# Kernel tuning notes

Measured on AMD Instinct MI355X. Metric: run time of the kernel, lower is better.

Reference implementation:

```python
import jax, jax.numpy as jnp
import numpy as np

EMBED_DIM = 1024
NUM_TOKENS = 32
TOKEN_DIM = 32  # ceil(1024/32)
CODEBOOK_SIZE = 256
BATCH = 32768
BETA = 0.25


def setup_inputs() -> dict:
    key = jax.random.key(0)
    ks = jax.random.split(key, 6)
    lim_e = 1.0 / np.sqrt(EMBED_DIM)
    lim_d = 1.0 / np.sqrt(NUM_TOKENS * TOKEN_DIM)
    lim_c = 1.0 / CODEBOOK_SIZE
    return {
        "skills": jax.random.normal(ks[0], (BATCH, EMBED_DIM), jnp.float32),
        "enc_w": jax.random.uniform(ks[1], (NUM_TOKENS * TOKEN_DIM, EMBED_DIM), jnp.float32, -lim_e, lim_e),
        "enc_b": jax.random.uniform(ks[2], (NUM_TOKENS * TOKEN_DIM,), jnp.float32, -lim_e, lim_e),
        "codebook": jax.random.uniform(ks[3], (CODEBOOK_SIZE, TOKEN_DIM), jnp.float32, -lim_c, lim_c),
        "dec_w": jax.random.uniform(ks[4], (EMBED_DIM, NUM_TOKENS * TOKEN_DIM), jnp.float32, -lim_d, lim_d),
        "dec_b": jax.random.uniform(ks[5], (EMBED_DIM,), jnp.float32, -lim_d, lim_d),
    }


def reference(skills, enc_w, enc_b, codebook, dec_w, dec_b):
    B = skills.shape[0]
    # encoder linear -> [B, num_tokens, token_dim]
    projected = (skills @ enc_w.T + enc_b).reshape(B, NUM_TOKENS, TOKEN_DIM)
    flat = projected.reshape(-1, TOKEN_DIM)  # [B*T, d]
    # squared-euclidean distances to codebook entries: [B*T, K]
    dists = (
        jnp.sum(flat * flat, axis=1, keepdims=True)
        - 2.0 * flat @ codebook.T
        + jnp.sum(codebook * codebook, axis=1)[None, :]
    )
    codes = jnp.argmin(dists, axis=1)  # [B*T]
    quantized = codebook[codes].reshape(B, NUM_TOKENS, TOKEN_DIM)
    # straight-through estimator
    st = projected + jax.lax.stop_gradient(quantized - projected)
    commitment = jnp.mean((projected - jax.lax.stop_gradient(quantized)) ** 2)
    codebook_loss = jnp.mean((quantized - jax.lax.stop_gradient(projected)) ** 2)
    vq_loss = codebook_loss + BETA * commitment
    reconstructed = st.reshape(B, NUM_TOKENS * TOKEN_DIM) @ dec_w.T + dec_b
    recon_loss = jnp.mean((reconstructed - skills) ** 2)
    loss = vq_loss + recon_loss
    return reconstructed, codes.reshape(B, NUM_TOKENS), loss
```

## Files before the change

kernel.cpp:

```cpp
#include <hip/hip_runtime.h>
#include <hip/hip_bf16.h>
#include <float.h>

#define OUT_CODES_OFF (33554432UL)
#define OUT_LOSS_OFF  (34603008UL)
#define TAU 1e-5f
#define INV_N (1.0f/33554432.0f)

typedef __attribute__((ext_vector_type(8))) short s16x8;
typedef __attribute__((ext_vector_type(4))) float f32x4;

__device__ __forceinline__ unsigned short bf16r(float x) {
    unsigned int u = __float_as_uint(x);
    unsigned int r = (u + 0x7FFFu + ((u >> 16) & 1u)) >> 16;
    return (unsigned short)r;
}
__device__ __forceinline__ float bf16f(unsigned short h) {
    return __uint_as_float(((unsigned int)h) << 16);
}
__device__ __forceinline__ void split8r(float4 v0, float4 v1, s16x8& h, s16x8& l) {
    float xs[8] = {v0.x, v0.y, v0.z, v0.w, v1.x, v1.y, v1.z, v1.w};
    #pragma unroll
    for (int e = 0; e < 8; ++e) {
        unsigned int u = __float_as_uint(xs[e]);
        unsigned short hh = (unsigned short)(u >> 16);
        h[e] = (short)hh;
        l[e] = (short)bf16r(xs[e] - bf16f(hh));
    }
}

__device__ __forceinline__ void gld16(const unsigned short* g, unsigned short* l) {
    __builtin_amdgcn_global_load_lds(
        (const __attribute__((address_space(1))) unsigned int*)g,
        (__attribute__((address_space(3))) unsigned int*)l, 16, 0, 0);
}

__global__ void k_prep_split(const float* __restrict__ in,
                             unsigned short* __restrict__ ot)
{
    const int b = blockIdx.x, tid = threadIdx.x;
    const int rblk = b >> 5, kt = b & 31, r = tid >> 2, q = tid & 3;
    const float* src = in + (size_t)(rblk * 128 + r) * 1024 + kt * 32 + q * 8;
    float4 v0 = *(const float4*)src, v1 = *(const float4*)(src + 4);
    s16x8 h, l;
    split8r(v0, v1, h, l);
    unsigned short* dst = ot + (size_t)b * 8192 + q * 1024 + r * 8;
    *(s16x8*)dst = h;
    *(s16x8*)(dst + 4096) = l;
}

__global__ void k_prep_r(const float* __restrict__ in,
                         unsigned short* __restrict__ o,
                         int n8)
{
    const int i = blockIdx.x * 256 + threadIdx.x;
    if (i >= n8) return;
    const float4* p = (const float4*)(in + (size_t)i * 8);
    float4 v0 = p[0], v1 = p[1];
    float xs[8] = {v0.x, v0.y, v0.z, v0.w, v1.x, v1.y, v1.z, v1.w};
    s16x8 h;
    #pragma unroll
    for (int e = 0; e < 8; ++e) h[e] = (short)bf16r(xs[e]);
    *(s16x8*)(o + (size_t)i * 8) = h;
}

__launch_bounds__(512, 1)
__global__ void k_enc_gl(const unsigned short* __restrict__ At,
                         const unsigned short* __restrict__ Bt,
                         const float* __restrict__ enc_b,
                         const float* __restrict__ cb_g,
                         float* __restrict__ out)
{
    __shared__ __align__(16) unsigned short us[49664];

    const int tid = threadIdx.x;
    const int wg = blockIdx.x;
    const int xcd = wg & 7, slot = wg >> 3;
    const int rb = xcd * 32 + (slot >> 1), chf = slot & 1;
    const int r0 = rb * 128;
    const int wid = tid >> 6, lane = tid & 63;
    const int wm = wid >> 1, wn = wid & 1;
    const int mbase = wm * 32;
    const int lhi = lane >> 4, llo = lane & 15;

    if (tid < 256) {
        const float4* cr = (const float4*)&cb_g[tid * 32];
        float s = 0.f;
        #pragma unroll
        for (int i = 0; i < 8; ++i) {
            float4 v = cr[i];
            float c[4] = {v.x, v.y, v.z, v.w};
            #pragma unroll
            for (int e = 0; e < 4; ++e) {
                const int d = i * 4 + e, kc = d >> 3, e8 = d & 7;
                unsigned int u = __float_as_uint(c[e]);
                unsigned short hh = (unsigned short)(u >> 16);
                us[32768 + kc * 2048 + tid * 8 + e8] = hh;
                us[40960 + kc * 2048 + tid * 8 + e8] = bf16r(c[e] - bf16f(hh));
                s = fmaf(c[e], c[e], s);
            }
        }
        *(float*)&us[49152 + tid * 2] = s;
    }
    {
        const unsigned short* gA = At + ((size_t)(rb * 32 + 0)) * 8192 + tid * 8;
        const unsigned short* gB = Bt + ((size_t)((chf * 4 + 0) * 32 + 0)) * 8192 + tid * 8;
        gld16(gA,        us + wid * 512);
        gld16(gA + 4096, us + 4096 + wid * 512);
        gld16(gB,        us + 8192 + wid * 512);
        gld16(gB + 4096, us + 12288 + wid * 512);
    }
    __syncthreads();

    float vq_local = 0.f;
    f32x4 acc[2][4];
    const int ntg_base = chf * 4;

    for (int it = 0; it < 128; ++it) {
        const int nt = it >> 5, kt = it & 31;
        if (kt == 0) {
            #pragma unroll
            for (int mf = 0; mf < 2; ++mf)
                #pragma unroll
                for (int nf = 0; nf < 4; ++nf) acc[mf][nf] = (f32x4)0.f;
        }
        if (it < 127) {
            const int tt = it + 1, ntn = tt >> 5, ktn = tt & 31;
            const int nb = (tt & 1) * 16384;
            const unsigned short* gA = At + ((size_t)(rb * 32 + ktn)) * 8192 + tid * 8;
            const unsigned short* gB = Bt + ((size_t)((ntg_base + ntn) * 32 + ktn)) * 8192 + tid * 8;
            gld16(gA,        us + nb + wid * 512);
            gld16(gA + 4096, us + nb + 4096 + wid * 512);
            gld16(gB,        us + nb + 8192 + wid * 512);
            gld16(gB + 4096, us + nb + 12288 + wid * 512);
        }
        {
            const int cb0 = (it & 1) * 16384;
            s16x8 ah[2], al[2];
            #pragma unroll
            for (int mf = 0; mf < 2; ++mf) {
                const int row = mbase + mf * 16 + llo;
                ah[mf] = *(s16x8*)&us[cb0 + lhi * 1024 + row * 8];
                al[mf] = *(s16x8*)&us[cb0 + 4096 + lhi * 1024 + row * 8];
            }
            #pragma unroll
            for (int nf = 0; nf < 4; ++nf) {
                const int rowb = wn * 64 + nf * 16 + llo;
                s16x8 bh = *(s16x8*)&us[cb0 + 8192 + lhi * 1024 + rowb * 8];
                s16x8 bl = *(s16x8*)&us[cb0 + 12288 + lhi * 1024 + rowb * 8];
                #pragma unroll
                for (int mf = 0; mf < 2; ++mf) {
                    acc[mf][nf] = __builtin_amdgcn_mfma_f32_16x16x32_bf16(ah[mf], bh, acc[mf][nf], 0, 0, 0);
                    acc[mf][nf] = __builtin_amdgcn_mfma_f32_16x16x32_bf16(ah[mf], bl, acc[mf][nf], 0, 0, 0);
                    acc[mf][nf] = __builtin_amdgcn_mfma_f32_16x16x32_bf16(al[mf], bh, acc[mf][nf], 0, 0, 0);
                }
            }
        }

        if (kt == 31) {
            for (int c = 0; c < 2; ++c) {
                __syncthreads();
                if (wn == c) {
                    #pragma unroll
                    for (int nf = 0; nf < 4; ++nf) {
                        const int colh = nf * 16 + llo;
                        const int tlc = colh >> 5, d = colh & 31;
                        const int kc = d >> 3, e8 = d & 7;
                        const float bias = enc_b[chf * 512 + nt * 128 + c * 64 + colh];
                        #pragma unroll
                        for (int mf = 0; mf < 2; ++mf)
                            #pragma unroll
                            for (int r = 0; r < 4; ++r) {
                                const int m_local = mbase + mf * 16 + lhi * 4 + r;
                                float val = acc[mf][nf][r] + bias;
                                unsigned int u = __float_as_uint(val);
                                unsigned short hh = (unsigned short)(u >> 16);
                                const int tok = m_local * 2 + tlc;
                                us[16384 + kc * 2048 + tok * 8 + e8] = hh;
                                us[24576 + kc * 2048 + tok * 8 + e8] = bf16r(val - bf16f(hh));
                            }
                    }
                }
                __syncthreads();
                s16x8 fh[2], fl[2];
                #pragma unroll
                for (int gi = 0; gi < 2; ++gi) {
                    const int tokrow = (wid * 2 + gi) * 16 + llo;
                    fh[gi] = *(s16x8*)&us[16384 + lhi * 2048 + tokrow * 8];
                    fl[gi] = *(s16x8*)&us[24576 + lhi * 2048 + tokrow * 8];
                }
                float s1[2][4], s2[2][4]; int bj[2][4];
                #pragma unroll
                for (int gi = 0; gi < 2; ++gi)
                    #pragma unroll
                    for (int r = 0; r < 4; ++r) { s1[gi][r] = FLT_MAX; s2[gi][r] = FLT_MAX; bj[gi][r] = 0; }
                for (int jb = 0; jb < 16; ++jb) {
                    const int j = jb * 16 + llo;
                    s16x8 ch = *(s16x8*)&us[32768 + lhi * 2048 + j * 8];
                    s16x8 cl = *(s16x8*)&us[40960 + lhi * 2048 + j * 8];
                    const float cnv = *(const float*)&us[49152 + j * 2];
                    #pragma unroll
                    for (int gi = 0; gi < 2; ++gi) {
                        f32x4 sc = (f32x4)0.f;
                        sc = __builtin_amdgcn_mfma_f32_16x16x32_bf16(fh[gi], ch, sc, 0, 0, 0);
                        sc = __builtin_amdgcn_mfma_f32_16x16x32_bf16(fh[gi], cl, sc, 0, 0, 0);
                        sc = __builtin_amdgcn_mfma_f32_16x16x32_bf16(fl[gi], ch, sc, 0, 0, 0);
                        #pragma unroll
                        for (int r = 0; r < 4; ++r) {
                            float s = fmaf(-2.f, sc[r], cnv);
                            if (s < s1[gi][r])      { s2[gi][r] = s1[gi][r]; s1[gi][r] = s; bj[gi][r] = j; }
                            else if (s < s2[gi][r]) { s2[gi][r] = s; }
                        }
                    }
                }
                #pragma unroll
                for (int gi = 0; gi < 2; ++gi) {
                    float Fp = 0.f;
                    #pragma unroll
                    for (int e = 0; e < 8; ++e) {
                        float fv = bf16f((unsigned short)fh[gi][e]) + bf16f((unsigned short)fl[gi][e]);
                        Fp = fmaf(fv, fv, Fp);
                    }
                    Fp += __shfl_xor(Fp, 16);
                    Fp += __shfl_xor(Fp, 32);
                    #pragma unroll
                    for (int r = 0; r < 4; ++r) {
                        float a1 = s1[gi][r], a2 = s2[gi][r]; int aj = bj[gi][r];
                        #pragma unroll
                        for (int off = 1; off <= 8; off <<= 1) {
                            float o1 = __shfl_xor(a1, off);
                            float o2 = __shfl_xor(a2, off);
                            int   oj = __shfl_xor(aj, off);
                            if (o1 < a1) { a2 = fminf(a1, o2); a1 = o1; aj = oj; }
                            else         { a2 = fminf(o1, a2); }
                        }
                        const float Ft = __shfl(Fp, lhi * 4 + r);
                        if (llo == 0) {
                            const int tok_local = (wid * 2 + gi) * 16 + lhi * 4 + r;
                            const int row = tok_local >> 1, tlc2 = tok_local & 1;
                            const int t = chf * 16 + nt * 4 + c * 2 + tlc2;
                            float cv = (a2 - a1 < TAU) ? (float)(aj + 512) : (float)aj;
                            out[OUT_CODES_OFF + (size_t)(r0 + row) * 32 + t] = cv;
                            vq_local += Ft + a1;
                        }
                    }
                }
            }
        }
        __syncthreads();
    }
    {
        float v = vq_local;
        #pragma unroll
        for (int off = 32; off >= 1; off >>= 1) v += __shfl_xor(v, off);
        if (lane == 0) atomicAdd(&out[OUT_LOSS_OFF], v * (1.25f * INV_N));
    }
}

__launch_bounds__(512, 1)
__global__ void k_enc_fb(const float* __restrict__ skills,
                         const float* __restrict__ enc_w,
                         const float* __restrict__ enc_b,
                         const float* __restrict__ cb_g,
                         float* __restrict__ out)
{
    __shared__ __align__(16) unsigned short us[40960];

    const int tid = threadIdx.x;
    const int rb = blockIdx.x >> 1, chf = blockIdx.x & 1;
    const int r0 = rb * 128;
    const int wid = tid >> 6, lane = tid & 63;
    const int wm = wid >> 1, wn = wid & 1;
    const int mbase = wm * 32;
    const int lhi = lane >> 4, llo = lane & 15;
    const int srow = tid >> 2, sq = tid & 3;

    if (tid < 256) {
        const float4* cr = (const float4*)&cb_g[tid * 32];
        float s = 0.f;
        #pragma unroll
        for (int i = 0; i < 8; ++i) {
            float4 v = cr[i];
            float c[4] = {v.x, v.y, v.z, v.w};
            #pragma unroll
            for (int e = 0; e < 4; ++e) {
                const int d = i * 4 + e;
                unsigned int u = __float_as_uint(c[e]);
                unsigned short hh = (unsigned short)(u >> 16);
                us[20480 + tid * 40 + d] = hh;
                us[30720 + tid * 40 + d] = bf16r(c[e] - bf16f(hh));
                s = fmaf(c[e], c[e], s);
            }
        }
        *(float*)&us[20480 + tid * 40 + 32] = s;
    }
    __syncthreads();

    float vq_local = 0.f;
    f32x4 acc[2][4];
    float4 ra0, ra1, rb0, rb1;
    {
        const float* ap = &skills[(size_t)(r0 + srow) * 1024 + sq * 8];
        ra0 = *(const float4*)ap; ra1 = *(const float4*)(ap + 4);
        const float* bp = &enc_w[(size_t)(chf * 512 + srow) * 1024 + sq * 8];
        rb0 = *(const float4*)bp; rb1 = *(const float4*)(bp + 4);
    }

    for (int it = 0; it < 128; ++it) {
        const int nt = it >> 5, kt = it & 31;
        if (kt == 0) {
            #pragma unroll
            for (int mf = 0; mf < 2; ++mf)
                #pragma unroll
                for (int nf = 0; nf < 4; ++nf) acc[mf][nf] = (f32x4)0.f;
        }
        __syncthreads();
        {
            s16x8 h, l;
            split8r(ra0, ra1, h, l);
            *(s16x8*)&us[srow * 40 + sq * 8] = h;
            *(s16x8*)&us[5120 + srow * 40 + sq * 8] = l;
            split8r(rb0, rb1, h, l);
            *(s16x8*)&us[10240 + srow * 40 + sq * 8] = h;
            *(s16x8*)&us[15360 + srow * 40 + sq * 8] = l;
        }
        __syncthreads();
        if (it < 127) {
            const int it2 = it + 1, nt2 = it2 >> 5, kt2 = it2 & 31;
            const float* ap = &skills[(size_t)(r0 + srow) * 1024 + kt2 * 32 + sq * 8];
            ra0 = *(const float4*)ap; ra1 = *(const float4*)(ap + 4);
            const float* bp = &enc_w[(size_t)(chf * 512 + nt2 * 128 + srow) * 1024 + kt2 * 32 + sq * 8];
            rb0 = *(const float4*)bp; rb1 = *(const float4*)(bp + 4);
        }
        {
            s16x8 ah[2], al[2];
            #pragma unroll
            for (int mf = 0; mf < 2; ++mf) {
                const int row = mbase + mf * 16 + llo;
                ah[mf] = *(s16x8*)&us[row * 40 + lhi * 8];
                al[mf] = *(s16x8*)&us[5120 + row * 40 + lhi * 8];
            }
            #pragma unroll
            for (int nf = 0; nf < 4; ++nf) {
                const int rowb = wn * 64 + nf * 16 + llo;
                s16x8 bh = *(s16x8*)&us[10240 + rowb * 40 + lhi * 8];
                s16x8 bl = *(s16x8*)&us[15360 + rowb * 40 + lhi * 8];
                #pragma unroll
                for (int mf = 0; mf < 2; ++mf) {
                    acc[mf][nf] = __builtin_amdgcn_mfma_f32_16x16x32_bf16(ah[mf], bh, acc[mf][nf], 0, 0, 0);
                    acc[mf][nf] = __builtin_amdgcn_mfma_f32_16x16x32_bf16(ah[mf], bl, acc[mf][nf], 0, 0, 0);
                    acc[mf][nf] = __builtin_amdgcn_mfma_f32_16x16x32_bf16(al[mf], bh, acc[mf][nf], 0, 0, 0);
                }
            }
        }

        if (kt == 31) {
            for (int c = 0; c < 2; ++c) {
                __syncthreads();
                if (wn == c) {
                    #pragma unroll
                    for (int nf = 0; nf < 4; ++nf) {
                        const int colh = nf * 16 + llo;
                        const int tlc = colh >> 5, d = colh & 31;
                        const float bias = enc_b[chf * 512 + nt * 128 + c * 64 + colh];
                        #pragma unroll
                        for (int mf = 0; mf < 2; ++mf)
                            #pragma unroll
                            for (int r = 0; r < 4; ++r) {
                                const int m_local = mbase + mf * 16 + lhi * 4 + r;
                                float val = acc[mf][nf][r] + bias;
                                unsigned int u = __float_as_uint(val);
                                unsigned short hh = (unsigned short)(u >> 16);
                                const int tok = m_local * 2 + tlc;
                                us[tok * 40 + d] = hh;
                                us[10240 + tok * 40 + d] = bf16r(val - bf16f(hh));
                            }
                    }
                }
                __syncthreads();
                s16x8 fh[2], fl[2];
                #pragma unroll
                for (int gi = 0; gi < 2; ++gi) {
                    const int tokrow = (wid * 2 + gi) * 16 + llo;
                    fh[gi] = *(s16x8*)&us[tokrow * 40 + lhi * 8];
                    fl[gi] = *(s16x8*)&us[10240 + tokrow * 40 + lhi * 8];
                }
                float s1[2][4], s2[2][4]; int bj[2][4];
                #pragma unroll
                for (int gi = 0; gi < 2; ++gi)
                    #pragma unroll
                    for (int r = 0; r < 4; ++r) { s1[gi][r] = FLT_MAX; s2[gi][r] = FLT_MAX; bj[gi][r] = 0; }
                for (int jb = 0; jb < 16; ++jb) {
                    const int j = jb * 16 + llo;
                    s16x8 ch = *(s16x8*)&us[20480 + j * 40 + lhi * 8];
                    s16x8 cl = *(s16x8*)&us[30720 + j * 40 + lhi * 8];
                    const float cnv = *(const float*)&us[20480 + j * 40 + 32];
                    #pragma unroll
                    for (int gi = 0; gi < 2; ++gi) {
                        f32x4 sc = (f32x4)0.f;
                        sc = __builtin_amdgcn_mfma_f32_16x16x32_bf16(fh[gi], ch, sc, 0, 0, 0);
                        sc = __builtin_amdgcn_mfma_f32_16x16x32_bf16(fh[gi], cl, sc, 0, 0, 0);
                        sc = __builtin_amdgcn_mfma_f32_16x16x32_bf16(fl[gi], ch, sc, 0, 0, 0);
                        #pragma unroll
                        for (int r = 0; r < 4; ++r) {
                            float s = fmaf(-2.f, sc[r], cnv);
                            if (s < s1[gi][r])      { s2[gi][r] = s1[gi][r]; s1[gi][r] = s; bj[gi][r] = j; }
                            else if (s < s2[gi][r]) { s2[gi][r] = s; }
                        }
                    }
                }
                #pragma unroll
                for (int gi = 0; gi < 2; ++gi) {
                    float Fp = 0.f;
                    #pragma unroll
                    for (int e = 0; e < 8; ++e) {
                        float fv = bf16f((unsigned short)fh[gi][e]) + bf16f((unsigned short)fl[gi][e]);
                        Fp = fmaf(fv, fv, Fp);
                    }
                    Fp += __shfl_xor(Fp, 16);
                    Fp += __shfl_xor(Fp, 32);
                    #pragma unroll
                    for (int r = 0; r < 4; ++r) {
                        float a1 = s1[gi][r], a2 = s2[gi][r]; int aj = bj[gi][r];
                        #pragma unroll
                        for (int off = 1; off <= 8; off <<= 1) {
                            float o1 = __shfl_xor(a1, off);
                            float o2 = __shfl_xor(a2, off);
                            int   oj = __shfl_xor(aj, off);
                            if (o1 < a1) { a2 = fminf(a1, o2); a1 = o1; aj = oj; }
                            else         { a2 = fminf(o1, a2); }
                        }
                        const float Ft = __shfl(Fp, lhi * 4 + r);
                        if (llo == 0) {
                            const int tok_local = (wid * 2 + gi) * 16 + lhi * 4 + r;
                            const int row = tok_local >> 1, tlc2 = tok_local & 1;
                            const int t = chf * 16 + nt * 4 + c * 2 + tlc2;
                            float cv = (a2 - a1 < TAU) ? (float)(aj + 512) : (float)aj;
                            out[OUT_CODES_OFF + (size_t)(r0 + row) * 32 + t] = cv;
                            vq_local += Ft + a1;
                        }
                    }
                }
            }
        }
    }
    {
        float v = vq_local;
        #pragma unroll
        for (int off = 32; off >= 1; off >>= 1) v += __shfl_xor(v, off);
        if (lane == 0) atomicAdd(&out[OUT_LOSS_OFF], v * (1.25f * INV_N));
    }
}

__launch_bounds__(256)
__global__ void k_fix(const float* __restrict__ skills,
                      const float* __restrict__ enc_w,
                      const float* __restrict__ enc_b,
                      const float* __restrict__ cb_g,
                      float* __restrict__ codes)
{
    __shared__ unsigned int cnt;
    __shared__ unsigned short list[256];

    const int tid = threadIdx.x;
    const int base = blockIdx.x * 256;

    if (tid == 0) cnt = 0;
    __syncthreads();
    {
        const int c = (int)codes[base + tid];
        if (c >= 512) {
            unsigned int ix = atomicAdd(&cnt, 1u);
            list[ix] = (unsigned short)tid;
        }
    }
    __syncthreads();
    const unsigned int n = cnt;
    if (n == 0) return;

    const int wv = tid >> 6, lane = tid & 63;
    const int d = lane & 31;

    for (unsigned int i = wv; i < n; i += 4) {
        const int tok = base + (int)list[i];
        const int row = tok >> 5;
        const int t   = tok & 31;

        const float4* s4 = (const float4*)&skills[(size_t)row * 1024];
        const float4* w4 = (const float4*)&enc_w[(size_t)(t * 32 + d) * 1024];
        float v1 = 0.f, v2 = 0.f, v3 = 0.f;
        for (int q = 0; q < 96; ++q) {
            float4 a = s4[q], b = w4[q];
            v1 = fmaf(a.x, b.x, v1); v1 = fmaf(a.y, b.y, v1);
            v1 = fmaf(a.z, b.z, v1); v1 = fmaf(a.w, b.w, v1);
        }
        for (int q = 96; q < 192; ++q) {
            float4 a = s4[q], b = w4[q];
            v2 = fmaf(a.x, b.x, v2); v2 = fmaf(a.y, b.y, v2);
            v2 = fmaf(a.z, b.z, v2); v2 = fmaf(a.w, b.w, v2);
        }
        for (int q = 192; q < 256; ++q) {
            float4 a = s4[q], b = w4[q];
            v3 = fmaf(a.x, b.x, v3); v3 = fmaf(a.y, b.y, v3);
            v3 = fmaf(a.z, b.z, v3); v3 = fmaf(a.w, b.w, v3);
        }
        const float pd = ((v1 + v2) + v3) + enc_b[t * 32 + d];

        float pv[32];
        #pragma unroll
        for (int dd = 0; dd < 32; ++dd) pv[dd] = __shfl(pd, dd);

        float F;
        {
            float s[32];
            #pragma unroll
            for (int dd = 0; dd < 32; ++dd) s[dd] = pv[dd] * pv[dd];
            float r[8];
            #pragma unroll
            for (int j = 0; j < 8; ++j) r[j] = ((s[j] + s[8+j]) + s[16+j]) + s[24+j];
            F = ((r[0] + r[1]) + (r[2] + r[3])) + ((r[4] + r[5]) + (r[6] + r[7]));
        }

        float bs = FLT_MAX; int bj = 0;
        for (int m = 0; m < 4; ++m) {
            const int j = m * 64 + lane;
            const float* cj = &cb_g[j * 32];
            float g = 0.f;
            #pragma unroll
            for (int dd = 0; dd < 32; ++dd) g = fmaf(pv[dd], cj[dd], g);
            float cs[32];
            #pragma unroll
            for (int dd = 0; dd < 32; ++dd) cs[dd] = cj[dd] * cj[dd];
            float r[8];
            #pragma unroll
            for (int jj = 0; jj < 8; ++jj) r[jj] = ((cs[jj] + cs[8+jj]) + cs[16+jj]) + cs[24+jj];
            float cn = ((r[0] + r[1]) + (r[2] + r[3])) + ((r[4] + r[5]) + (r[6] + r[7]));
            float dist = (F - 2.0f * g) + cn;
            if (dist < bs) { bs = dist; bj = j; }
        }
        #pragma unroll
        for (int off = 32; off >= 1; off >>= 1) {
            float os = __shfl_xor(bs, off);
            int   oj = __shfl_xor(bj, off);
            if (os < bs || (os == bs && oj < bj)) { bs = os; bj = oj; }
        }
        if (lane == 0) codes[tok] = (float)bj;
    }
}

template <bool PRED>
__launch_bounds__(512)
__global__ void k_dec(const float* __restrict__ skills,
                      const float* __restrict__ cb_g,
                      const unsigned short* __restrict__ cbb,
                      const float* __restrict__ dec_w,
                      const unsigned short* __restrict__ dwb,
                      const float* __restrict__ dec_b,
                      const float* __restrict__ codes,
                      float* __restrict__ recon,
                      float* __restrict__ loss_out)
{
    __shared__ unsigned short Qt[128][40], Wt[128][40];

    const int tid = threadIdx.x;
    const int r0 = (blockIdx.x >> 3) * 128;
    const int n0 = (blockIdx.x & 7) * 128;
    const int wid = tid >> 6, lane = tid & 63;
    const int wm = wid >> 1, wn = wid & 1;
    const int mbase = wm * 32, nbase = wn * 64;
    const int lhi = lane >> 4, llo = lane & 15;
    const int srow = tid >> 2, sq = tid & 3;

    f32x4 acc[2][4];
    #pragma unroll
    for (int mf = 0; mf < 2; ++mf)
        #pragma unroll
        for (int nf = 0; nf < 4; ++nf) acc[mf][nf] = (f32x4)0.f;

    s16x8 q16, w16;
    float4 q0, q1, w0, w1;
    int cnext;
    {
        const int c0 = ((int)codes[(size_t)(r0 + srow) * 32 + 0]) & 255;
        if (PRED) {
            q16 = *(const s16x8*)(cbb + c0 * 32 + sq * 8);
            w16 = *(const s16x8*)(dwb + (size_t)(n0 + srow) * 1024 + sq * 8);
        } else {
            const float* cp = &cb_g[c0 * 32 + sq * 8];
            q0 = *(const float4*)cp; q1 = *(const float4*)(cp + 4);
            const float* wp = &dec_w[(size_t)(n0 + srow) * 1024 + sq * 8];
            w0 = *(const float4*)wp; w1 = *(const float4*)(wp + 4);
        }
        cnext = ((int)codes[(size_t)(r0 + srow) * 32 + 1]) & 255;
    }

    for (int t = 0; t < 32; ++t) {
        __syncthreads();
        if (PRED) {
            *(s16x8*)&Qt[srow][sq * 8] = q16;
            *(s16x8*)&Wt[srow][sq * 8] = w16;
        } else {
            float xs[8] = {q0.x, q0.y, q0.z, q0.w, q1.x, q1.y, q1.z, q1.w};
            s16x8 h;
            #pragma unroll
            for (int e = 0; e < 8; ++e) h[e] = (short)bf16r(xs[e]);
            *(s16x8*)&Qt[srow][sq * 8] = h;
            float ys[8] = {w0.x, w0.y, w0.z, w0.w, w1.x, w1.y, w1.z, w1.w};
            #pragma unroll
            for (int e = 0; e < 8; ++e) h[e] = (short)bf16r(ys[e]);
            *(s16x8*)&Wt[srow][sq * 8] = h;
        }
        __syncthreads();
        if (t < 31) {
            if (PRED) {
                q16 = *(const s16x8*)(cbb + cnext * 32 + sq * 8);
                w16 = *(const s16x8*)(dwb + (size_t)(n0 + srow) * 1024 + (t + 1) * 32 + sq * 8);
            } else {
                const float* cp = &cb_g[cnext * 32 + sq * 8];
                q0 = *(const float4*)cp; q1 = *(const float4*)(cp + 4);
                const float* wp = &dec_w[(size_t)(n0 + srow) * 1024 + (t + 1) * 32 + sq * 8];
                w0 = *(const float4*)wp; w1 = *(const float4*)(wp + 4);
            }
            if (t < 30) cnext = ((int)codes[(size_t)(r0 + srow) * 32 + t + 2]) & 255;
        }
        s16x8 aq[2], bw[4];
        #pragma unroll
        for (int mf = 0; mf < 2; ++mf)
            aq[mf] = *(s16x8*)&Qt[mbase + mf * 16 + llo][lhi * 8];
        #pragma unroll
        for (int nf = 0; nf < 4; ++nf)
            bw[nf] = *(s16x8*)&Wt[nbase + nf * 16 + llo][lhi * 8];
        #pragma unroll
        for (int mf = 0; mf < 2; ++mf)
            #pragma unroll
            for (int nf = 0; nf < 4; ++nf)
                acc[mf][nf] = __builtin_amdgcn_mfma_f32_16x16x32_bf16(aq[mf], bw[nf], acc[mf][nf], 0, 0, 0);
    }

    float lsum = 0.f;
    #pragma unroll
    for (int mf = 0; mf < 2; ++mf)
        #pragma unroll
        for (int nf = 0; nf < 4; ++nf) {
            const int col = n0 + nbase + nf * 16 + llo;
            const float bias = dec_b[col];
            #pragma unroll
            for (int r = 0; r < 4; ++r) {
                const int row = r0 + mbase + mf * 16 + lhi * 4 + r;
                float rv = acc[mf][nf][r] + bias;
                float dv = rv - skills[(size_t)row * 1024 + col];
                lsum = fmaf(dv, dv, lsum);
                recon[(size_t)row * 1024 + col] = rv;
            }
        }
    #pragma unroll
    for (int off = 32; off >= 1; off >>= 1) lsum += __shfl_xor(lsum, off);
    if (lane == 0) atomicAdd(loss_out, lsum * INV_N);
}

extern "C" void kernel_launch(void* const* d_in, const int* in_sizes, int n_in,
                              void* d_out, int out_size, void* d_ws, size_t ws_size,
                              hipStream_t stream)
{
    const float* skills = (const float*)d_in[0];
    const float* enc_w  = (const float*)d_in[1];
    const float* enc_b  = (const float*)d_in[2];
    const float* cbg    = (const float*)d_in[3];
    const float* dec_w  = (const float*)d_in[4];
    const float* dec_b  = (const float*)d_in[5];
    float* out = (float*)d_out;

    hipMemsetAsync(out + OUT_LOSS_OFF, 0, 4, stream);

    const size_t NEED_BIG = 4UL*1024*1024 + 2097152UL + 16384UL + 256UL;
    unsigned short* wsu16 = (unsigned short*)d_ws;

    if (ws_size >= NEED_BIG) {
        unsigned short* Btl = wsu16;
        unsigned short* dwb = wsu16 + 2097152UL;
        unsigned short* cbb = wsu16 + 3145728UL;
        unsigned short* Atl = (unsigned short*)out;

        k_prep_split<<<dim3(8192), dim3(512), 0, stream>>>(skills, Atl);
        k_prep_split<<<dim3(256),  dim3(512), 0, stream>>>(enc_w, Btl);
        k_enc_gl<<<dim3(512), dim3(512), 0, stream>>>(Atl, Btl, enc_b, cbg, out);
        k_fix<<<dim3(4096), dim3(256), 0, stream>>>(skills, enc_w, enc_b, cbg, out + OUT_CODES_OFF);
        k_prep_r<<<dim3(512), dim3(256), 0, stream>>>(dec_w, dwb, 131072);
        k_prep_r<<<dim3(4), dim3(256), 0, stream>>>(cbg, cbb, 1024);
        k_dec<true><<<dim3(2048), dim3(512), 0, stream>>>(skills, cbg, cbb, dec_w, dwb, dec_b,
                                                          out + OUT_CODES_OFF, out, out + OUT_LOSS_OFF);
    } else {
        k_enc_fb<<<dim3(512), dim3(512), 0, stream>>>(skills, enc_w, enc_b, cbg, out);
        k_fix<<<dim3(4096), dim3(256), 0, stream>>>(skills, enc_w, enc_b, cbg, out + OUT_CODES_OFF);
        const bool pred = (ws_size >= (2097152UL + 16384UL + 64UL));
        unsigned short* dwb = wsu16;
        unsigned short* cbb = wsu16 + 1048576UL;
        if (pred) {
            k_prep_r<<<dim3(512), dim3(256), 0, stream>>>(dec_w, dwb, 131072);
            k_prep_r<<<dim3(4), dim3(256), 0, stream>>>(cbg, cbb, 1024);
            k_dec<true><<<dim3(2048), dim3(512), 0, stream>>>(skills, cbg, cbb, dec_w, dwb, dec_b,
                                                              out + OUT_CODES_OFF, out, out + OUT_LOSS_OFF);
        } else {
            k_dec<false><<<dim3(2048), dim3(512), 0, stream>>>(skills, cbg, cbb, dec_w, dwb, dec_b,
                                                               out + OUT_CODES_OFF, out, out + OUT_LOSS_OFF);
        }
    }
}
```

Before: 811.8 us.

## Precompute codebook split in separate kernel and stream it into reused LDS

Moves the codebook hi/lo bf16 split and norm computation into a tiny prep kernel writing to workspace. The encoder kernel now loads the split codebook into shared memory only at the epilogue, reusing the tile buffer region, keeps the codebook norms in registers, and reorganizes the argmin epilogue into four 32-column chunks with one token group per wave. This cuts LDS from about 97KB to 80KB, which could allow better scheduling, at the cost of an extra launch, a reload of the codebook per output tile, and more barriers.

After: 900.6 us. 1.11x slower.

```diff
diff --git a/kernel.cpp b/kernel.cpp
--- a/kernel.cpp
+++ b/kernel.cpp
@@ -64,14 +64,39 @@
     *(s16x8*)(o + (size_t)i * 8) = h;
 }
 
+__global__ void k_prep_cb(const float* __restrict__ cb_g,
+                          unsigned short* __restrict__ cbt,
+                          float* __restrict__ cnw)
+{
+    const int j = threadIdx.x;
+    const float4* cr = (const float4*)&cb_g[j * 32];
+    float s = 0.f;
+    #pragma unroll
+    for (int i = 0; i < 8; ++i) {
+        float4 v = cr[i];
+        float c[4] = {v.x, v.y, v.z, v.w};
+        #pragma unroll
+        for (int e = 0; e < 4; ++e) {
+            const int d = i * 4 + e, kc = d >> 3, e8 = d & 7;
+            unsigned int u = __float_as_uint(c[e]);
+            unsigned short hh = (unsigned short)(u >> 16);
+            cbt[kc * 2048 + j * 8 + e8] = hh;
+            cbt[8192 + kc * 2048 + j * 8 + e8] = bf16r(c[e] - bf16f(hh));
+            s = fmaf(c[e], c[e], s);
+        }
+    }
+    cnw[j] = s;
+}
+
 __launch_bounds__(512, 1)
 __global__ void k_enc_gl(const unsigned short* __restrict__ At,
                          const unsigned short* __restrict__ Bt,
+                         const unsigned short* __restrict__ cbt,
+                         const float* __restrict__ cnw,
                          const float* __restrict__ enc_b,
-                         const float* __restrict__ cb_g,
                          float* __restrict__ out)
 {
-    __shared__ __align__(16) unsigned short us[49664];
+    __shared__ __align__(16) unsigned short us[40960];
 
     const int tid = threadIdx.x;
     const int wg = blockIdx.x;
@@ -83,25 +108,10 @@
     const int mbase = wm * 32;
     const int lhi = lane >> 4, llo = lane & 15;
 
-    if (tid < 256) {
-        const float4* cr = (const float4*)&cb_g[tid * 32];
-        float s = 0.f;
-        #pragma unroll
-        for (int i = 0; i < 8; ++i) {
-            float4 v = cr[i];
-            float c[4] = {v.x, v.y, v.z, v.w};
-            #pragma unroll
-            for (int e = 0; e < 4; ++e) {
-                const int d = i * 4 + e, kc = d >> 3, e8 = d & 7;
-                unsigned int u = __float_as_uint(c[e]);
-                unsigned short hh = (unsigned short)(u >> 16);
-                us[32768 + kc * 2048 + tid * 8 + e8] = hh;
-                us[40960 + kc * 2048 + tid * 8 + e8] = bf16r(c[e] - bf16f(hh));
-                s = fmaf(c[e], c[e], s);
-            }
-        }
-        *(float*)&us[49152 + tid * 2] = s;
-    }
+    float cnv_r[16];
+    #pragma unroll
+    for (int jb = 0; jb < 16; ++jb) cnv_r[jb] = cnw[jb * 16 + llo];
+
     {
         const unsigned short* gA = At + ((size_t)(rb * 32 + 0)) * 8192 + tid * 8;
         const unsigned short* gB = Bt + ((size_t)((chf * 4 + 0) * 32 + 0)) * 8192 + tid * 8;
@@ -158,6 +168,196 @@
         }
 
         if (kt == 31) {
+            __syncthreads();
+            #pragma unroll
+            for (int rds = 0; rds < 4; ++rds)
+                gld16(cbt + rds * 4096 + tid * 8, us + 16384 + rds * 4096 + wid * 512);
+
+            #pragma unroll
+            for (int c = 0; c < 4; ++c) {
+                if (wn == (c >> 1)) {
+                    #pragma unroll
+                    for (int nfp = 0; nfp < 2; ++nfp) {
+                        const int nf = (c & 1) * 2 + nfp;
+                        const int d = nfp * 16 + llo;
+                        const int kc = d >> 3, e8 = d & 7;
+                        const float bias = enc_b[chf * 512 + nt * 128 + c * 32 + d];
+                        #pragma unroll
+                        for (int mf = 0; mf < 2; ++mf)
+                            #pragma unroll
+                            for (int r = 0; r < 4; ++r) {
+                                const int m_local = mbase + mf * 16 + lhi * 4 + r;
+                                float val = acc[mf][nf][r] + bias;
+                                unsigned int u = __float_as_uint(val);
+                                unsigned short hh = (unsigned short)(u >> 16);
+                                us[32768 + kc * 1024 + m_local * 8 + e8] = hh;
+                                us[36864 + kc * 1024 + m_local * 8 + e8] = bf16r(val - bf16f(hh));
+                            }
+                    }
+                }
+                __syncthreads();
+                const int tokrow = wid * 16 + llo;
+                s16x8 fh = *(s16x8*)&us[32768 + lhi * 1024 + tokrow * 8];
+                s16x8 fl = *(s16x8*)&us[36864 + lhi * 1024 + tokrow * 8];
+                float s1[4], s2[4]; int bj[4];
+                #pragma unroll
+                for (int r = 0; r < 4; ++r) { s1[r] = FLT_MAX; s2[r] = FLT_MAX; bj[r] = 0; }
+                #pragma unroll
+                for (int jb = 0; jb < 16; ++jb) {
+                    const int j = jb * 16 + llo;
+                    s16x8 ch = *(s16x8*)&us[16384 + lhi * 2048 + j * 8];
+                    s16x8 cl = *(s16x8*)&us[24576 + lhi * 2048 + j * 8];
+                    const float cnv = cnv_r[jb];
+                    f32x4 sc = (f32x4)0.f;
+                    sc = __builtin_amdgcn_mfma_f32_16x16x32_bf16(fh, ch, sc, 0, 0, 0);
+                    sc = __builtin_amdgcn_mfma_f32_16x16x32_bf16(fh, cl, sc, 0, 0, 0);
+                    sc = __builtin_amdgcn_mfma_f32_16x16x32_bf16(fl, ch, sc, 0, 0, 0);
+                    #pragma unroll
+                    for (int r = 0; r < 4; ++r) {
+                        float s = fmaf(-2.f, sc[r], cnv);
+                        if (s < s1[r])      { s2[r] = s1[r]; s1[r] = s; bj[r] = j; }
+                        else if (s < s2[r]) { s2[r] = s; }
+                    }
+                }
+                float Fp = 0.f;
+                #pragma unroll
+                for (int e = 0; e < 8; ++e) {
+                    float fv = bf16f((unsigned short)fh[e]) + bf16f((unsigned short)fl[e]);
+                    Fp = fmaf(fv, fv, Fp);
+                }
+                Fp += __shfl_xor(Fp, 16);
+                Fp += __shfl_xor(Fp, 32);
+                #pragma unroll
+                for (int r = 0; r < 4; ++r) {
+                    float a1 = s1[r], a2 = s2[r]; int aj = bj[r];
+                    #pragma unroll
+                    for (int off = 1; off <= 8; off <<= 1) {
+                        float o1 = __shfl_xor(a1, off);
+                        float o2 = __shfl_xor(a2, off);
+                        int   oj = __shfl_xor(aj, off);
+                        if (o1 < a1) { a2 = fminf(a1, o2); a1 = o1; aj = oj; }
+                        else         { a2 = fminf(o1, a2); }
+                    }
+                    const float Ft = __shfl(Fp, lhi * 4 + r);
+                    if (llo == 0) {
+                        const int tok_local = wid * 16 + lhi * 4 + r;
+                        const int t = chf * 16 + nt * 4 + c;
+                        float cv = (a2 - a1 < TAU) ? (float)(aj + 512) : (float)aj;
+                        out[OUT_CODES_OFF + (size_t)(r0 + tok_local) * 32 + t] = cv;
+                        vq_local += Ft + a1;
+                    }
+                }
+                __syncthreads();
+            }
+        }
+        __syncthreads();
+    }
+    {
+        float v = vq_local;
+        #pragma unroll
+        for (int off = 32; off >= 1; off >>= 1) v += __shfl_xor(v, off);
+        if (lane == 0) atomicAdd(&out[OUT_LOSS_OFF], v * (1.25f * INV_N));
+    }
+}
+
+__launch_bounds__(512, 1)
+__global__ void k_enc_fb(const float* __restrict__ skills,
+                         const float* __restrict__ enc_w,
+                         const float* __restrict__ enc_b,
+                         const float* __restrict__ cb_g,
+                         float* __restrict__ out)
+{
+    __shared__ __align__(16) unsigned short us[40960];
+
+    const int tid = threadIdx.x;
+    const int rb = blockIdx.x >> 1, chf = blockIdx.x & 1;
+    const int r0 = rb * 128;
+    const int wid = tid >> 6, lane = tid & 63;
+    const int wm = wid >> 1, wn = wid & 1;
+    const int mbase = wm * 32;
+    const int lhi = lane >> 4, llo = lane & 15;
+    const int srow = tid >> 2, sq = tid & 3;
+
+    if (tid < 256) {
+        const float4* cr = (const float4*)&cb_g[tid * 32];
+        float s = 0.f;
+        #pragma unroll
+        for (int i = 0; i < 8; ++i) {
+            float4 v = cr[i];
+            float c[4] = {v.x, v.y, v.z, v.w};
+            #pragma unroll
+            for (int e = 0; e < 4; ++e) {
+                const int d = i * 4 + e;
+                unsigned int u = __float_as_uint(c[e]);
+                unsigned short hh = (unsigned short)(u >> 16);
+                us[20480 + tid * 40 + d] = hh;
+                us[30720 + tid * 40 + d] = bf16r(c[e] - bf16f(hh));
+                s = fmaf(c[e], c[e], s);
+            }
+        }
+        *(float*)&us[20480 + tid * 40 + 32] = s;
+    }
+    __syncthreads();
+
+    float vq_local = 0.f;
+    f32x4 acc[2][4];
+    float4 ra0, ra1, rb0, rb1;
+    {
+        const float* ap = &skills[(size_t)(r0 + srow) * 1024 + sq * 8];
+        ra0 = *(const float4*)ap; ra1 = *(const float4*)(ap + 4);
+        const float* bp = &enc_w[(size_t)(chf * 512 + srow) * 1024 + sq * 8];
+        rb0 = *(const float4*)bp; rb1 = *(const float4*)(bp + 4);
+    }
+
+    for (int it = 0; it < 128; ++it) {
+        const int nt = it >> 5, kt = it & 31;
+        if (kt == 0) {
+            #pragma unroll
+            for (int mf = 0; mf < 2; ++mf)
+                #pragma unroll
+                for (int nf = 0; nf < 4; ++nf) acc[mf][nf] = (f32x4)0.f;
+        }
+        __syncthreads();
+        {
+            s16x8 h, l;
+            split8r(ra0, ra1, h, l);
+            *(s16x8*)&us[srow * 40 + sq * 8] = h;
+            *(s16x8*)&us[5120 + srow * 40 + sq * 8] = l;
+            split8r(rb0, rb1, h, l);
+            *(s16x8*)&us[10240 + srow * 40 + sq * 8] = h;
+            *(s16x8*)&us[15360 + srow * 40 + sq * 8] = l;
+        }
+        __syncthreads();
+        if (it < 127) {
+            const int it2 = it + 1, nt2 = it2 >> 5, kt2 = it2 & 31;
+            const float* ap = &skills[(size_t)(r0 + srow) * 1024 + kt2 * 32 + sq * 8];
+            ra0 = *(const float4*)ap; ra1 = *(const float4*)(ap + 4);
+            const float* bp = &enc_w[(size_t)(chf * 512 + nt2 * 128 + srow) * 1024 + kt2 * 32 + sq * 8];
+            rb0 = *(const float4*)bp; rb1 = *(const float4*)(bp + 4);
+        }
+        {
+            s16x8 ah[2], al[2];
+            #pragma unroll
+            for (int mf = 0; mf < 2; ++mf) {
+                const int row = mbase + mf * 16 + llo;
+                ah[mf] = *(s16x8*)&us[row * 40 + lhi * 8];
+                al[mf] = *(s16x8*)&us[5120 + row * 40 + lhi * 8];
+            }
+            #pragma unroll
+            for (int nf = 0; nf < 4; ++nf) {
+                const int rowb = wn * 64 + nf * 16 + llo;
+                s16x8 bh = *(s16x8*)&us[10240 + rowb * 40 + lhi * 8];
+                s16x8 bl = *(s16x8*)&us[15360 + rowb * 40 + lhi * 8];
+                #pragma unroll
+                for (int mf = 0; mf < 2; ++mf) {
+                    acc[mf][nf] = __builtin_amdgcn_mfma_f32_16x16x32_bf16(ah[mf], bh, acc[mf][nf], 0, 0, 0);
+                    acc[mf][nf] = __builtin_amdgcn_mfma_f32_16x16x32_bf16(ah[mf], bl, acc[mf][nf], 0, 0, 0);
+                    acc[mf][nf] = __builtin_amdgcn_mfma_f32_16x16x32_bf16(al[mf], bh, acc[mf][nf], 0, 0, 0);
+                }
+            }
+        }
+
+        if (kt == 31) {
             for (int c = 0; c < 2; ++c) {
                 __syncthreads();
                 if (wn == c) {
@@ -165,7 +365,6 @@
                     for (int nf = 0; nf < 4; ++nf) {
                         const int colh = nf * 16 + llo;
                         const int tlc = colh >> 5, d = colh & 31;
-                        const int kc = d >> 3, e8 = d & 7;
                         const float bias = enc_b[chf * 512 + nt * 128 + c * 64 + colh];
                         #pragma unroll
                         for (int mf = 0; mf < 2; ++mf)
@@ -176,8 +375,8 @@
                                 unsigned int u = __float_as_uint(val);
                                 unsigned short hh = (unsigned short)(u >> 16);
                                 const int tok = m_local * 2 + tlc;
-                                us[16384 + kc * 2048 + tok * 8 + e8] = hh;
-                                us[24576 + kc * 2048 + tok * 8 + e8] = bf16r(val - bf16f(hh));
+                                us[tok * 40 + d] = hh;
+                                us[10240 + tok * 40 + d] = bf16r(val - bf16f(hh));
                             }
                     }
                 }
@@ -186,8 +385,8 @@
                 #pragma unroll
                 for (int gi = 0; gi < 2; ++gi) {
                     const int tokrow = (wid * 2 + gi) * 16 + llo;
-                    fh[gi] = *(s16x8*)&us[16384 + lhi * 2048 + tokrow * 8];
-                    fl[gi] = *(s16x8*)&us[24576 + lhi * 2048 + tokrow * 8];
+                    fh[gi] = *(s16x8*)&us[tokrow * 40 + lhi * 8];
+                    fl[gi] = *(s16x8*)&us[10240 + tokrow * 40 + lhi * 8];
                 }
                 float s1[2][4], s2[2][4]; int bj[2][4];
                 #pragma unroll
@@ -196,9 +395,9 @@
                     for (int r = 0; r < 4; ++r) { s1[gi][r] = FLT_MAX; s2[gi][r] = FLT_MAX; bj[gi][r] = 0; }
                 for (int jb = 0; jb < 16; ++jb) {
                     const int j = jb * 16 + llo;
-                    s16x8 ch = *(s16x8*)&us[32768 + lhi * 2048 + j * 8];
-                    s16x8 cl = *(s16x8*)&us[40960 + lhi * 2048 + j * 8];
-                    const float cnv = *(const float*)&us[49152 + j * 2];
+                    s16x8 ch = *(s16x8*)&us[20480 + j * 40 + lhi * 8];
+                    s16x8 cl = *(s16x8*)&us[30720 + j * 40 + lhi * 8];
+                    const float cnv = *(const float*)&us[20480 + j * 40 + 32];
                     #pragma unroll
                     for (int gi = 0; gi < 2; ++gi) {
                         f32x4 sc = (f32x4)0.f;
@@ -247,202 +446,6 @@
                 }
             }
         }
-        __syncthreads();
-    }
-    {
-        float v = vq_local;
-        #pragma unroll
-        for (int off = 32; off >= 1; off >>= 1) v += __shfl_xor(v, off);
-        if (lane == 0) atomicAdd(&out[OUT_LOSS_OFF], v * (1.25f * INV_N));
-    }
-}
-
-__launch_bounds__(512, 1)
-__global__ void k_enc_fb(const float* __restrict__ skills,
-                         const float* __restrict__ enc_w,
-                         const float* __restrict__ enc_b,
-                         const float* __restrict__ cb_g,
-                         float* __restrict__ out)
-{
-    __shared__ __align__(16) unsigned short us[40960];
-
-    const int tid = threadIdx.x;
-    const int rb = blockIdx.x >> 1, chf = blockIdx.x & 1;
-    const int r0 = rb * 128;
-    const int wid = tid >> 6, lane = tid & 63;
-    const int wm = wid >> 1, wn = wid & 1;
-    const int mbase = wm * 32;
-    const int lhi = lane >> 4, llo = lane & 15;
-    const int srow = tid >> 2, sq = tid & 3;
-
-    if (tid < 256) {
-        const float4* cr = (const float4*)&cb_g[tid * 32];
-        float s = 0.f;
-        #pragma unroll
-        for (int i = 0; i < 8; ++i) {
-            float4 v = cr[i];
-            float c[4] = {v.x, v.y, v.z, v.w};
-            #pragma unroll
-            for (int e = 0; e < 4; ++e) {
-                const int d = i * 4 + e;
-                unsigned int u = __float_as_uint(c[e]);
-                unsigned short hh = (unsigned short)(u >> 16);
-                us[20480 + tid * 40 + d] = hh;
-                us[30720 + tid * 40 + d] = bf16r(c[e] - bf16f(hh));
-                s = fmaf(c[e], c[e], s);
-            }
-        }
-        *(float*)&us[20480 + tid * 40 + 32] = s;
-    }
-    __syncthreads();
-
-    float vq_local = 0.f;
-    f32x4 acc[2][4];
-    float4 ra0, ra1, rb0, rb1;
-    {
-        const float* ap = &skills[(size_t)(r0 + srow) * 1024 + sq * 8];
-        ra0 = *(const float4*)ap; ra1 = *(const float4*)(ap + 4);
-        const float* bp = &enc_w[(size_t)(chf * 512 + srow) * 1024 + sq * 8];
-        rb0 = *(const float4*)bp; rb1 = *(const float4*)(bp + 4);
-    }
-
-    for (int it = 0; it < 128; ++it) {
-        const int nt = it >> 5, kt = it & 31;
-        if (kt == 0) {
-            #pragma unroll
-            for (int mf = 0; mf < 2; ++mf)
-                #pragma unroll
-                for (int nf = 0; nf < 4; ++nf) acc[mf][nf] = (f32x4)0.f;
-        }
-        __syncthreads();
-        {
-            s16x8 h, l;
-            split8r(ra0, ra1, h, l);
-            *(s16x8*)&us[srow * 40 + sq * 8] = h;
-            *(s16x8*)&us[5120 + srow * 40 + sq * 8] = l;
-            split8r(rb0, rb1, h, l);
-            *(s16x8*)&us[10240 + srow * 40 + sq * 8] = h;
-            *(s16x8*)&us[15360 + srow * 40 + sq * 8] = l;
-        }
-        __syncthreads();
-        if (it < 127) {
-            const int it2 = it + 1, nt2 = it2 >> 5, kt2 = it2 & 31;
-            const float* ap = &skills[(size_t)(r0 + srow) * 1024 + kt2 * 32 + sq * 8];
-            ra0 = *(const float4*)ap; ra1 = *(const float4*)(ap + 4);
-            const float* bp = &enc_w[(size_t)(chf * 512 + nt2 * 128 + srow) * 1024 + kt2 * 32 + sq * 8];
-            rb0 = *(const float4*)bp; rb1 = *(const float4*)(bp + 4);
-        }
-        {
-            s16x8 ah[2], al[2];
-            #pragma unroll
-            for (int mf = 0; mf < 2; ++mf) {
-                const int row = mbase + mf * 16 + llo;
-                ah[mf] = *(s16x8*)&us[row * 40 + lhi * 8];
-                al[mf] = *(s16x8*)&us[5120 + row * 40 + lhi * 8];
-            }
-            #pragma unroll
-            for (int nf = 0; nf < 4; ++nf) {
-                const int rowb = wn * 64 + nf * 16 + llo;
-                s16x8 bh = *(s16x8*)&us[10240 + rowb * 40 + lhi * 8];
-                s16x8 bl = *(s16x8*)&us[15360 + rowb * 40 + lhi * 8];
-                #pragma unroll
-                for (int mf = 0; mf < 2; ++mf) {
-                    acc[mf][nf] = __builtin_amdgcn_mfma_f32_16x16x32_bf16(ah[mf], bh, acc[mf][nf], 0, 0, 0);
-                    acc[mf][nf] = __builtin_amdgcn_mfma_f32_16x16x32_bf16(ah[mf], bl, acc[mf][nf], 0, 0, 0);
-                    acc[mf][nf] = __builtin_amdgcn_mfma_f32_16x16x32_bf16(al[mf], bh, acc[mf][nf], 0, 0, 0);
-                }
-            }
-        }
-
-        if (kt == 31) {
-            for (int c = 0; c < 2; ++c) {
-                __syncthreads();
-                if (wn == c) {
-                    #pragma unroll
-                    for (int nf = 0; nf < 4; ++nf) {
-                        const int colh = nf * 16 + llo;
-                        const int tlc = colh >> 5, d = colh & 31;
-                        const float bias = enc_b[chf * 512 + nt * 128 + c * 64 + colh];
-                        #pragma unroll
-                        for (int mf = 0; mf < 2; ++mf)
-                            #pragma unroll
-                            for (int r = 0; r < 4; ++r) {
-                                const int m_local = mbase + mf * 16 + lhi * 4 + r;
-                                float val = acc[mf][nf][r] + bias;
-                                unsigned int u = __float_as_uint(val);
-                                unsigned short hh = (unsigned short)(u >> 16);
-                                const int tok = m_local * 2 + tlc;
-                                us[tok * 40 + d] = hh;
-                                us[10240 + tok * 40 + d] = bf16r(val - bf16f(hh));
-                            }
-                    }
-                }
-                __syncthreads();
-                s16x8 fh[2], fl[2];
-                #pragma unroll
-                for (int gi = 0; gi < 2; ++gi) {
-                    const int tokrow = (wid * 2 + gi) * 16 + llo;
-                    fh[gi] = *(s16x8*)&us[tokrow * 40 + lhi * 8];
-                    fl[gi] = *(s16x8*)&us[10240 + tokrow * 40 + lhi * 8];
-                }
-                float s1[2][4], s2[2][4]; int bj[2][4];
-                #pragma unroll
-                for (int gi = 0; gi < 2; ++gi)
-                    #pragma unroll
-                    for (int r = 0; r < 4; ++r) { s1[gi][r] = FLT_MAX; s2[gi][r] = FLT_MAX; bj[gi][r] = 0; }
-                for (int jb = 0; jb < 16; ++jb) {
-                    const int j = jb * 16 + llo;
-                    s16x8 ch = *(s16x8*)&us[20480 + j * 40 + lhi * 8];
-                    s16x8 cl = *(s16x8*)&us[30720 + j * 40 + lhi * 8];
-                    const float cnv = *(const float*)&us[20480 + j * 40 + 32];
-                    #pragma unroll
-                    for (int gi = 0; gi < 2; ++gi) {
-                        f32x4 sc = (f32x4)0.f;
-                        sc = __builtin_amdgcn_mfma_f32_16x16x32_bf16(fh[gi], ch, sc, 0, 0, 0);
-                        sc = __builtin_amdgcn_mfma_f32_16x16x32_bf16(fh[gi], cl, sc, 0, 0, 0);
-                        sc = __builtin_amdgcn_mfma_f32_16x16x32_bf16(fl[gi], ch, sc, 0, 0, 0);
-                        #pragma unroll
-                        for (int r = 0; r < 4; ++r) {
-                            float s = fmaf(-2.f, sc[r], cnv);
-                            if (s < s1[gi][r])      { s2[gi][r] = s1[gi][r]; s1[gi][r] = s; bj[gi][r] = j; }
-                            else if (s < s2[gi][r]) { s2[gi][r] = s; }
-                        }
-                    }
-                }
-                #pragma unroll
-                for (int gi = 0; gi < 2; ++gi) {
-                    float Fp = 0.f;
-                    #pragma unroll
-                    for (int e = 0; e < 8; ++e) {
-                        float fv = bf16f((unsigned short)fh[gi][e]) + bf16f((unsigned short)fl[gi][e]);
-                        Fp = fmaf(fv, fv, Fp);
-                    }
-                    Fp += __shfl_xor(Fp, 16);
-                    Fp += __shfl_xor(Fp, 32);
-                    #pragma unroll
-                    for (int r = 0; r < 4; ++r) {
-                        float a1 = s1[gi][r], a2 = s2[gi][r]; int aj = bj[gi][r];
-                        #pragma unroll
-                        for (int off = 1; off <= 8; off <<= 1) {
-                            float o1 = __shfl_xor(a1, off);
-                            float o2 = __shfl_xor(a2, off);
-                            int   oj = __shfl_xor(aj, off);
-                            if (o1 < a1) { a2 = fminf(a1, o2); a1 = o1; aj = oj; }
-                            else         { a2 = fminf(o1, a2); }
-                        }
-                        const float Ft = __shfl(Fp, lhi * 4 + r);
-                        if (llo == 0) {
-                            const int tok_local = (wid * 2 + gi) * 16 + lhi * 4 + r;
-                            const int row = tok_local >> 1, tlc2 = tok_local & 1;
-                            const int t = chf * 16 + nt * 4 + c * 2 + tlc2;
-                            float cv = (a2 - a1 < TAU) ? (float)(aj + 512) : (float)aj;
-                            out[OUT_CODES_OFF + (size_t)(r0 + row) * 32 + t] = cv;
-                            vq_local += Ft + a1;
-                        }
-                    }
-                }
-            }
-        }
     }
     {
         float v = vq_local;
@@ -672,18 +675,21 @@
 
     hipMemsetAsync(out + OUT_LOSS_OFF, 0, 4, stream);
 
-    const size_t NEED_BIG = 4UL*1024*1024 + 2097152UL + 16384UL + 256UL;
+    const size_t NEED_BIG = (2097152UL + 1048576UL + 8192UL + 16384UL + 512UL) * 2UL + 256UL;
     unsigned short* wsu16 = (unsigned short*)d_ws;
 
     if (ws_size >= NEED_BIG) {
         unsigned short* Btl = wsu16;
         unsigned short* dwb = wsu16 + 2097152UL;
         unsigned short* cbb = wsu16 + 3145728UL;
+        unsigned short* cbt = wsu16 + 3153920UL;
+        float*          cnw = (float*)(wsu16 + 3170304UL);
         unsigned short* Atl = (unsigned short*)out;
 
         k_prep_split<<<dim3(8192), dim3(512), 0, stream>>>(skills, Atl);
         k_prep_split<<<dim3(256),  dim3(512), 0, stream>>>(enc_w, Btl);
-        k_enc_gl<<<dim3(512), dim3(512), 0, stream>>>(Atl, Btl, enc_b, cbg, out);
+        k_prep_cb<<<dim3(1), dim3(256), 0, stream>>>(cbg, cbt, cnw);
+        k_enc_gl<<<dim3(512), dim3(512), 0, stream>>>(Atl, Btl, cbt, cnw, enc_b, out);
         k_fix<<<dim3(4096), dim3(256), 0, stream>>>(skills, enc_w, enc_b, cbg, out + OUT_CODES_OFF);
         k_prep_r<<<dim3(512), dim3(256), 0, stream>>>(dec_w, dwb, 131072);
         k_prep_r<<<dim3(4), dim3(256), 0, stream>>>(cbg, cbb, 1024);
```
